# Optimization experiments

Hardware: AMD Instinct MI355X
Metric: run time of the kernel (lower is better)

## Reference

```python
import jax, jax.numpy as jnp
import numpy as np

D = 16          # input_dim
H = 64          # hidden per tiny h-model
HG = 64 * D     # hidden of joint g model = 1024
B = 32768       # batch


def _init_linear(key, out_dim, in_dim):
    # torch nn.Linear default init: U(-1/sqrt(in), 1/sqrt(in)) for W and b
    kw, kb = jax.random.split(key)
    bound = 1.0 / np.sqrt(in_dim)
    W = jax.random.uniform(kw, (out_dim, in_dim), minval=-bound, maxval=bound, dtype=jnp.float32)
    b = jax.random.uniform(kb, (out_dim,), minval=-bound, maxval=bound, dtype=jnp.float32)
    return W, b


def setup_inputs() -> dict:
    key = jax.random.key(0)
    keys = jax.random.split(key, 16)
    x = jax.random.normal(keys[0], (B, 2 * D), dtype=jnp.float32)

    # Stacked weights for the D tiny h-models (1->64->64->64->64->1)
    def stack_h(k, out_dim, in_dim):
        ks = jax.random.split(k, D)
        Ws, bs = [], []
        for kk in ks:
            W, b = _init_linear(kk, out_dim, in_dim)
            Ws.append(W); bs.append(b)
        return jnp.stack(Ws), jnp.stack(bs)

    hW1, hb1 = stack_h(keys[1], H, 1)    # [D,64,1], [D,64]
    hW2, hb2 = stack_h(keys[2], H, H)    # [D,64,64]
    hW3, hb3 = stack_h(keys[3], H, H)
    hW4, hb4 = stack_h(keys[4], H, H)
    hW5, hb5 = stack_h(keys[5], 1, H)    # [D,1,64], [D,1]

    gW1, gb1 = _init_linear(keys[6], HG, D)
    gW2, gb2 = _init_linear(keys[7], HG, HG)
    gW3, gb3 = _init_linear(keys[8], HG, HG)
    gW4, gb4 = _init_linear(keys[9], HG, HG)
    gW5, gb5 = _init_linear(keys[10], 1, HG)

    return {
        "x": x,
        "hW1": hW1, "hb1": hb1, "hW2": hW2, "hb2": hb2,
        "hW3": hW3, "hb3": hb3, "hW4": hW4, "hb4": hb4,
        "hW5": hW5, "hb5": hb5,
        "gW1": gW1, "gb1": gb1, "gW2": gW2, "gb2": gb2,
        "gW3": gW3, "gb3": gb3, "gW4": gW4, "gb4": gb4,
        "gW5": gW5, "gb5": gb5,
    }


def reference(x, hW1, hb1, hW2, hb2, hW3, hb3, hW4, hb4, hW5, hb5,
              gW1, gb1, gW2, gb2, gW3, gb3, gW4, gb4, gW5, gb5):
    first_half = x[:, :D]    # [B, D] -> g branch
    second_half = x[:, D:]   # [B, D] -> D tiny h models, one scalar each

    # --- h branch: D independent 1->64->64->64->64->1 MLPs, batched ---
    # layer 1: scalar input per model; hW1[...,0] has shape [D, H]
    h = jax.nn.relu(second_half[:, :, None] * hW1[:, :, 0][None] + hb1[None])  # [B, D, H]
    h = jax.nn.relu(jnp.einsum('bdh,dgh->bdg', h, hW2) + hb2[None])            # [B, D, H]
    h = jax.nn.relu(jnp.einsum('bdh,dgh->bdg', h, hW3) + hb3[None])
    h = jax.nn.relu(jnp.einsum('bdh,dgh->bdg', h, hW4) + hb4[None])
    outputs_h = jnp.einsum('bdh,doh->bdo', h, hW5)[:, :, 0] + hb5[None, :, 0]  # [B, D]

    # --- g branch: D -> 64D -> ... -> 1 MLP ---
    g = jax.nn.relu(first_half @ gW1.T + gb1)  # [B, HG]
    g = jax.nn.relu(g @ gW2.T + gb2)
    g = jax.nn.relu(g @ gW3.T + gb3)
    g = jax.nn.relu(g @ gW4.T + gb4)
    outputs_g = g @ gW5.T + gb5                # [B, 1]

    return outputs_h, outputs_g
```

## Files before the change

### kernel.cpp

```cpp
#include <hip/hip_runtime.h>

#define B_ROWS 32768
#define D_NETS 16
#define MWH    1048576
#define GW1OFF (3 * MWH)
#define HPOFF  (GW1OFF + 16384)

typedef _Float16 half8 __attribute__((ext_vector_type(8)));
typedef _Float16 half4 __attribute__((ext_vector_type(4)));
typedef __attribute__((ext_vector_type(16))) float f32x16;

#define MFMA16 __builtin_amdgcn_mfma_f32_32x32x16_f16

__global__ void pack_f16(const float* __restrict__ gW1,
                         const float* __restrict__ gW2,
                         const float* __restrict__ gW3,
                         const float* __restrict__ gW4,
                         const float* __restrict__ hW2,
                         const float* __restrict__ hW3,
                         const float* __restrict__ hW4,
                         _Float16* __restrict__ ws) {
    const int p = blockIdx.x * 256 + threadIdx.x;
    const float* src;
    size_t dst;
    if (p < 393216) {
        const int lz = p >> 17;
        const int pl = p & 131071;
        const float* W = (lz == 0) ? gW2 : (lz == 1) ? gW3 : gW4;
        const int l = pl & 63, g = (pl >> 6) & 31, ks = pl >> 11;
        src = &W[(size_t)(g * 32 + (l & 31)) * 1024 + ks * 16 + (l >> 5) * 8];
        dst = (size_t)lz * MWH + (size_t)pl * 8;
    } else if (p < 395264) {
        const int q = p - 393216;
        const int l = q & 63, g = q >> 6;
        src = &gW1[(g * 32 + (l & 31)) * 16 + (l >> 5) * 8];
        dst = GW1OFF + (size_t)q * 8;
    } else {
        const int q = p - 395264;
        const int l = q & 63;
        const int sub = (q >> 6) & 7;
        const int ks = sub >> 1, g = sub & 1;
        const int dL = q >> 9;
        const int d = dL / 3, L = dL - d * 3;
        const float* W = (L == 0) ? hW2 : (L == 1) ? hW3 : hW4;
        src = &W[d * 4096 + (g * 32 + (l & 31)) * 64 + ks * 16 + (l >> 5) * 8];
        dst = HPOFF + (size_t)q * 8;
    }
    half8 v;
    #pragma unroll
    for (int kk = 0; kk < 8; ++kk) v[kk] = (_Float16)src[kk];
    *(half8*)&ws[dst] = v;
}

__global__ __launch_bounds__(256, 4) void h_net_mfma(
    const float* __restrict__ x,
    const float* __restrict__ hW1, const float* __restrict__ hb1,
    const float* __restrict__ hb2, const float* __restrict__ hb3,
    const float* __restrict__ hb4,
    const float* __restrict__ hW5, const float* __restrict__ hb5,
    const _Float16* __restrict__ ws,
    float* __restrict__ out)
{
    __shared__ _Float16 sA[8192];
    __shared__ float s_w1[64], s_b1[64], s_bs[3][64], s_w5[64];

    const int t = threadIdx.x;
    const int d = blockIdx.y;
    const int row0 = blockIdx.x * 128;
    const int l = t & 63, wv = t >> 6;
    const int l31 = l & 31, lk = l >> 5;

    if (t < 64) {
        s_w1[t]    = hW1[d * 64 + t];
        s_b1[t]    = hb1[d * 64 + t];
        s_bs[0][t] = hb2[d * 64 + t];
        s_bs[1][t] = hb3[d * 64 + t];
        s_bs[2][t] = hb4[d * 64 + t];
        s_w5[t]    = hW5[d * 64 + t];
    }
    __syncthreads();

    {
        const int row = t >> 1, jh = t & 1, rg = row >> 5, r31 = row & 31;
        const float sv = x[(size_t)(row0 + row) * 32 + 16 + d];
        #pragma unroll
        for (int jj = 0; jj < 32; ++jj) {
            const int j = jh * 32 + jj;
            const float a = fmaxf(fmaf(sv, s_w1[j], s_b1[j]), 0.f);
            const int ks = j >> 4;
            const int li = ((((j >> 3) & 1) << 5) | r31) ^ (ks << 3);
            sA[((rg * 4 + ks) * 64 + li) * 8 + (j & 7)] = (_Float16)a;
        }
    }
    __syncthreads();

    const _Float16* hp = ws + HPOFF + (size_t)d * 3 * 4096;

    #pragma unroll 1
    for (int L = 0; L < 3; ++L) {
        const _Float16* W = hp + (size_t)L * 4096;
        half8 B[4][2], A[4];
        #pragma unroll
        for (int ks = 0; ks < 4; ++ks) {
            B[ks][0] = *(const half8*)&W[((ks * 2 + 0) * 64 + l) * 8];
            B[ks][1] = *(const half8*)&W[((ks * 2 + 1) * 64 + l) * 8];
            A[ks] = *(const half8*)&sA[((wv * 4 + ks) * 64 + (l ^ (ks << 3))) * 8];
        }
        f32x16 acc[2];
        #pragma unroll
        for (int nt = 0; nt < 2; ++nt) {
            const float bv = s_bs[L][nt * 32 + l31];
            #pragma unroll
            for (int r = 0; r < 16; ++r) acc[nt][r] = bv;
        }
        #pragma unroll
        for (int ks = 0; ks < 4; ++ks) {
            acc[0] = MFMA16(A[ks], B[ks][0], acc[0], 0, 0, 0);
            acc[1] = MFMA16(A[ks], B[ks][1], acc[1], 0, 0, 0);
        }
        __syncthreads();
        #pragma unroll
        for (int nt = 0; nt < 2; ++nt) {
            #pragma unroll
            for (int r = 0; r < 16; ++r) {
                const int r31 = (r & 3) + 8 * (r >> 2) + 4 * lk;
                const int col = nt * 32 + l31;
                const float v = fmaxf(acc[nt][r], 0.f);
                const int ks = col >> 4;
                const int li = ((((col >> 3) & 1) << 5) | r31) ^ (ks << 3);
                sA[((wv * 4 + ks) * 64 + li) * 8 + (col & 7)] = (_Float16)v;
            }
        }
        __syncthreads();
    }

    {
        const int row = t >> 1, jh = t & 1, rg = row >> 5, r31 = row & 31;
        float s = 0.f;
        #pragma unroll
        for (int ks2 = 0; ks2 < 2; ++ks2) {
            const int ks = jh * 2 + ks2;
            #pragma unroll
            for (int h2 = 0; h2 < 2; ++h2) {
                const int li = ((h2 << 5) | r31) ^ (ks << 3);
                half8 v = *(const half8*)&sA[((rg * 4 + ks) * 64 + li) * 8];
                const float* w = &s_w5[ks * 16 + h2 * 8];
                #pragma unroll
                for (int kk = 0; kk < 8; ++kk)
                    s = fmaf((float)v[kk], w[kk], s);
            }
        }
        s += __shfl_xor(s, 1);
        if (jh == 0) out[(size_t)(row0 + row) * 16 + d] = s + hb5[d];
    }
}

__global__ __launch_bounds__(1024, 4) void g_fused_v3(
    const float* __restrict__ x,
    const _Float16* __restrict__ ws,
    const float* __restrict__ gb1, const float* __restrict__ gb2,
    const float* __restrict__ gb3, const float* __restrict__ gb4,
    const float* __restrict__ gW5, const float* __restrict__ gb5,
    float* __restrict__ out)
{
    __shared__ _Float16 sA[65536];
    __shared__ float s_w5f[1024];
    __shared__ float s_red[1024];

    const int t = threadIdx.x;
    const int l = t & 63, wv = t >> 6;
    const int l31 = l & 31, lk = l >> 5;
    const int n0 = wv * 64;
    const int row0 = blockIdx.x * 64;

    s_w5f[t] = gW5[t];

    f32x16 acc[2][2];

#define G_EPI()                                                              \
    {                                                                        \
        _Pragma("unroll")                                                    \
        for (int nt = 0; nt < 2; ++nt) {                                     \
            _Pragma("unroll")                                                \
            for (int rg = 0; rg < 2; ++rg) {                                 \
                _Pragma("unroll")                                            \
                for (int q = 0; q < 4; ++q) {                                \
                    half4 v;                                                 \
                    _Pragma("unroll")                                        \
                    for (int j = 0; j < 4; ++j)                              \
                        v[j] = (_Float16)fmaxf(acc[nt][rg][q * 4 + j], 0.f); \
                    const int ksn = wv * 4 + nt * 2 + (q >> 1);              \
                    const int li  = ((q & 1) << 5) | l31;                    \
                    *(half4*)&sA[((rg * 64 + ksn) * 64 + li) * 8 + lk * 4] = v; \
                }                                                            \
            }                                                                \
        }                                                                    \
    }

    {
        half8 xb[2];
        #pragma unroll
        for (int rg = 0; rg < 2; ++rg) {
            const float* xp = &x[(size_t)(row0 + rg * 32 + l31) * 32 + lk * 8];
            #pragma unroll
            for (int kk = 0; kk < 8; ++kk) xb[rg][kk] = (_Float16)xp[kk];
        }
        #pragma unroll
        for (int nt = 0; nt < 2; ++nt) {
            half8 wb = *(const half8*)&ws[GW1OFF + ((wv * 2 + nt) * 64 + l) * 8];
            #pragma unroll
            for (int rg = 0; rg < 2; ++rg) {
                #pragma unroll
                for (int r = 0; r < 16; ++r)
                    acc[nt][rg][r] =
                        gb1[n0 + nt * 32 + (r & 3) + 8 * (r >> 2) + 4 * lk];
                acc[nt][rg] = MFMA16(wb, xb[rg], acc[nt][rg], 0, 0, 0);
            }
        }
    }
    G_EPI();
    __syncthreads();

#define G_LA(ks, A_)                                                         \
    { A_[0] = *(const half8*)&sA[((ks) * 64 + l) * 8];                       \
      A_[1] = *(const half8*)&sA[((64 + (ks)) * 64 + l) * 8]; }
#define G_LB(ks, B_)                                                         \
    { const int _o = (ks) * 16384 + wv * 1024 + l * 8;                       \
      B_[0] = *(const half8*)&W[_o];                                         \
      B_[1] = *(const half8*)&W[_o + 512]; }
#define G_MM(A_, B_)                                                         \
    { acc[0][0] = MFMA16(B_[0], A_[0], acc[0][0], 0, 0, 0);                  \
      acc[0][1] = MFMA16(B_[0], A_[1], acc[0][1], 0, 0, 0);                  \
      acc[1][0] = MFMA16(B_[1], A_[0], acc[1][0], 0, 0, 0);                  \
      acc[1][1] = MFMA16(B_[1], A_[1], acc[1][1], 0, 0, 0); }

    #pragma unroll 1
    for (int L = 0; L < 3; ++L) {
        const _Float16* W = ws + (size_t)L * MWH;
        const float* gbL = (L == 0) ? gb2 : (L == 1) ? gb3 : gb4;

        half8 A0[2], A1[2], B0[2], B1[2];
        G_LA(0, A0); G_LB(0, B0);
        G_LA(1, A1); G_LB(1, B1);

        #pragma unroll
        for (int nt = 0; nt < 2; ++nt)
            #pragma unroll
            for (int rg = 0; rg < 2; ++rg)
                #pragma unroll
                for (int r = 0; r < 16; ++r)
                    acc[nt][rg][r] =
                        gbL[n0 + nt * 32 + (r & 3) + 8 * (r >> 2) + 4 * lk];

        #pragma unroll 1
        for (int ks = 0; ks < 64; ks += 2) {
            G_MM(A0, B0);
            if (ks + 2 < 64) { G_LA(ks + 2, A0); G_LB(ks + 2, B0); }
            G_MM(A1, B1);
            if (ks + 3 < 64) { G_LA(ks + 3, A1); G_LB(ks + 3, B1); }
        }

        __syncthreads();
        G_EPI();
        __syncthreads();
    }
#undef G_LA
#undef G_LB
#undef G_MM
#undef G_EPI

    {
        const int row = t & 63;
        const int rg5 = row >> 5, r31 = row & 31;
        const int c = t >> 6;
        float s = 0.f;
        #pragma unroll
        for (int q = 0; q < 4; ++q) {
            #pragma unroll
            for (int kh = 0; kh < 2; ++kh) {
                half8 v = *(const half8*)&sA[((rg5 * 64 + c * 4 + q) * 64 +
                                             ((kh << 5) | r31)) * 8];
                const float* w = &s_w5f[(c * 4 + q) * 16 + kh * 8];
                #pragma unroll
                for (int kk = 0; kk < 8; ++kk)
                    s = fmaf((float)v[kk], w[kk], s);
            }
        }
        s_red[t] = s;
    }
    __syncthreads();
    if (t < 64) {
        float s = gb5[0];
        #pragma unroll
        for (int c = 0; c < 16; ++c) s += s_red[c * 64 + t];
        out[(size_t)B_ROWS * D_NETS + row0 + t] = s;
    }
}

extern "C" void kernel_launch(void* const* d_in, const int* in_sizes, int n_in,
                              void* d_out, int out_size, void* d_ws, size_t ws_size,
                              hipStream_t stream) {
    (void)in_sizes; (void)n_in; (void)out_size; (void)ws_size;

    const float* x   = (const float*)d_in[0];
    const float* hW1 = (const float*)d_in[1];
    const float* hb1 = (const float*)d_in[2];
    const float* hW2 = (const float*)d_in[3];
    const float* hb2 = (const float*)d_in[4];
    const float* hW3 = (const float*)d_in[5];
    const float* hb3 = (const float*)d_in[6];
    const float* hW4 = (const float*)d_in[7];
    const float* hb4 = (const float*)d_in[8];
    const float* hW5 = (const float*)d_in[9];
    const float* hb5 = (const float*)d_in[10];
    const float* gW1 = (const float*)d_in[11];
    const float* gb1 = (const float*)d_in[12];
    const float* gW2 = (const float*)d_in[13];
    const float* gb2 = (const float*)d_in[14];
    const float* gW3 = (const float*)d_in[15];
    const float* gb3 = (const float*)d_in[16];
    const float* gW4 = (const float*)d_in[17];
    const float* gb4 = (const float*)d_in[18];
    const float* gW5 = (const float*)d_in[19];
    const float* gb5 = (const float*)d_in[20];
    float* out = (float*)d_out;
    _Float16* wsh = (_Float16*)d_ws;

    pack_f16<<<1640, 256, 0, stream>>>(gW1, gW2, gW3, gW4, hW2, hW3, hW4, wsh);

    dim3 gh(B_ROWS / 128, D_NETS);
    h_net_mfma<<<gh, 256, 0, stream>>>(x, hW1, hb1, hb2, hb3, hb4,
                                       hW5, hb5, wsh, out);

    g_fused_v3<<<B_ROWS / 64, 1024, 0, stream>>>(x, wsh, gb1, gb2, gb3, gb4,
                                                 gW5, gb5, out);
}
```

Measured before the change: 264.0 us.

## Halve g-kernel block to 512 threads with 128-column warp tiles and deeper prefetch

The fused g-MLP kernel now runs 8 waves per block instead of 16. Each wave owns 128 output columns, so it holds 4x2 MFMA accumulators, and each A fragment loaded from LDS feeds twice as many MFMAs. The K-loop becomes a 4-stage rotating register pipeline that prefetches B weights three steps ahead, with clamped indices to avoid branches. This cuts LDS traffic per MFMA and hides global weight-load latency, at the cost of more registers per thread and fewer waves to hide latency.

```diff
diff --git a/kernel.cpp b/kernel.cpp
--- a/kernel.cpp
+++ b/kernel.cpp
@@ -155,7 +155,7 @@
     }
 }
 
-__global__ __launch_bounds__(1024, 4) void g_fused_v3(
+__global__ __launch_bounds__(512, 2) void g_fused_v4(
     const float* __restrict__ x,
     const _Float16* __restrict__ ws,
     const float* __restrict__ gb1, const float* __restrict__ gb2,
@@ -165,22 +165,23 @@
 {
     __shared__ _Float16 sA[65536];
     __shared__ float s_w5f[1024];
-    __shared__ float s_red[1024];
+    __shared__ float s_red[512];
 
     const int t = threadIdx.x;
     const int l = t & 63, wv = t >> 6;
     const int l31 = l & 31, lk = l >> 5;
-    const int n0 = wv * 64;
+    const int n0 = wv * 128;
     const int row0 = blockIdx.x * 64;
 
     s_w5f[t] = gW5[t];
-
-    f32x16 acc[2][2];
+    s_w5f[t + 512] = gW5[t + 512];
+
+    f32x16 acc[4][2];
 
 #define G_EPI()                                                              \
     {                                                                        \
         _Pragma("unroll")                                                    \
-        for (int nt = 0; nt < 2; ++nt) {                                     \
+        for (int nt = 0; nt < 4; ++nt) {                                     \
             _Pragma("unroll")                                                \
             for (int rg = 0; rg < 2; ++rg) {                                 \
                 _Pragma("unroll")                                            \
@@ -189,7 +190,7 @@
                     _Pragma("unroll")                                        \
                     for (int j = 0; j < 4; ++j)                              \
                         v[j] = (_Float16)fmaxf(acc[nt][rg][q * 4 + j], 0.f); \
-                    const int ksn = wv * 4 + nt * 2 + (q >> 1);              \
+                    const int ksn = wv * 8 + nt * 2 + (q >> 1);              \
                     const int li  = ((q & 1) << 5) | l31;                    \
                     *(half4*)&sA[((rg * 64 + ksn) * 64 + li) * 8 + lk * 4] = v; \
                 }                                                            \
@@ -206,8 +207,8 @@
             for (int kk = 0; kk < 8; ++kk) xb[rg][kk] = (_Float16)xp[kk];
         }
         #pragma unroll
-        for (int nt = 0; nt < 2; ++nt) {
-            half8 wb = *(const half8*)&ws[GW1OFF + ((wv * 2 + nt) * 64 + l) * 8];
+        for (int nt = 0; nt < 4; ++nt) {
+            half8 wb = *(const half8*)&ws[GW1OFF + ((wv * 4 + nt) * 64 + l) * 8];
             #pragma unroll
             for (int rg = 0; rg < 2; ++rg) {
                 #pragma unroll
@@ -225,26 +226,31 @@
     { A_[0] = *(const half8*)&sA[((ks) * 64 + l) * 8];                       \
       A_[1] = *(const half8*)&sA[((64 + (ks)) * 64 + l) * 8]; }
 #define G_LB(ks, B_)                                                         \
-    { const int _o = (ks) * 16384 + wv * 1024 + l * 8;                       \
+    { const int _o = (ks) * 16384 + wv * 2048 + l * 8;                       \
       B_[0] = *(const half8*)&W[_o];                                         \
-      B_[1] = *(const half8*)&W[_o + 512]; }
+      B_[1] = *(const half8*)&W[_o + 512];                                   \
+      B_[2] = *(const half8*)&W[_o + 1024];                                  \
+      B_[3] = *(const half8*)&W[_o + 1536]; }
 #define G_MM(A_, B_)                                                         \
-    { acc[0][0] = MFMA16(B_[0], A_[0], acc[0][0], 0, 0, 0);                  \
-      acc[0][1] = MFMA16(B_[0], A_[1], acc[0][1], 0, 0, 0);                  \
-      acc[1][0] = MFMA16(B_[1], A_[0], acc[1][0], 0, 0, 0);                  \
-      acc[1][1] = MFMA16(B_[1], A_[1], acc[1][1], 0, 0, 0); }
+    { _Pragma("unroll")                                                      \
+      for (int nt = 0; nt < 4; ++nt) {                                       \
+          acc[nt][0] = MFMA16(B_[nt], A_[0], acc[nt][0], 0, 0, 0);           \
+          acc[nt][1] = MFMA16(B_[nt], A_[1], acc[nt][1], 0, 0, 0);           \
+      } }
 
     #pragma unroll 1
     for (int L = 0; L < 3; ++L) {
         const _Float16* W = ws + (size_t)L * MWH;
         const float* gbL = (L == 0) ? gb2 : (L == 1) ? gb3 : gb4;
 
-        half8 A0[2], A1[2], B0[2], B1[2];
-        G_LA(0, A0); G_LB(0, B0);
-        G_LA(1, A1); G_LB(1, B1);
-
-        #pragma unroll
-        for (int nt = 0; nt < 2; ++nt)
+        half8 A0[2], A1[2], A2[2], A3[2];
+        half8 B0[4], B1[4], B2[4], B3[4];
+
+        G_LB(0, B0); G_LB(1, B1); G_LB(2, B2);
+        G_LA(0, A0); G_LA(1, A1);
+
+        #pragma unroll
+        for (int nt = 0; nt < 4; ++nt)
             #pragma unroll
             for (int rg = 0; rg < 2; ++rg)
                 #pragma unroll
@@ -253,11 +259,17 @@
                         gbL[n0 + nt * 32 + (r & 3) + 8 * (r >> 2) + 4 * lk];
 
         #pragma unroll 1
-        for (int ks = 0; ks < 64; ks += 2) {
-            G_MM(A0, B0);
-            if (ks + 2 < 64) { G_LA(ks + 2, A0); G_LB(ks + 2, B0); }
-            G_MM(A1, B1);
-            if (ks + 3 < 64) { G_LA(ks + 3, A1); G_LB(ks + 3, B1); }
+        for (int ks = 0; ks < 64; ks += 4) {
+            int s2 = ks + 2; s2 = s2 > 63 ? 63 : s2;
+            int s3 = ks + 3; s3 = s3 > 63 ? 63 : s3;
+            int s4 = ks + 4; s4 = s4 > 63 ? 63 : s4;
+            int s5 = ks + 5; s5 = s5 > 63 ? 63 : s5;
+            int s6 = ks + 6; s6 = s6 > 63 ? 63 : s6;
+
+            G_LB(s3, B3);  G_LA(s2, A2);  G_MM(A0, B0);
+            G_LB(s4, B0);  G_LA(s3, A3);  G_MM(A1, B1);
+            G_LB(s5, B1);  G_LA(s4, A0);  G_MM(A2, B2);
+            G_LB(s6, B2);  G_LA(s5, A1);  G_MM(A3, B3);
         }
 
         __syncthreads();
@@ -270,17 +282,18 @@
 #undef G_EPI
 
     {
-        const int row = t & 63;
+        const int row = l;
         const int rg5 = row >> 5, r31 = row & 31;
-        const int c = t >> 6;
+        const int c = wv;
         float s = 0.f;
         #pragma unroll
-        for (int q = 0; q < 4; ++q) {
+        for (int q = 0; q < 8; ++q) {
+            const int ksn = c * 8 + q;
             #pragma unroll
             for (int kh = 0; kh < 2; ++kh) {
-                half8 v = *(const half8*)&sA[((rg5 * 64 + c * 4 + q) * 64 +
+                half8 v = *(const half8*)&sA[((rg5 * 64 + ksn) * 64 +
                                              ((kh << 5) | r31)) * 8];
-                const float* w = &s_w5f[(c * 4 + q) * 16 + kh * 8];
+                const float* w = &s_w5f[ksn * 16 + kh * 8];
                 #pragma unroll
                 for (int kk = 0; kk < 8; ++kk)
                     s = fmaf((float)v[kk], w[kk], s);
@@ -292,7 +305,7 @@
     if (t < 64) {
         float s = gb5[0];
         #pragma unroll
-        for (int c = 0; c < 16; ++c) s += s_red[c * 64 + t];
+        for (int c = 0; c < 8; ++c) s += s_red[c * 64 + t];
         out[(size_t)B_ROWS * D_NETS + row0 + t] = s;
     }
 }
@@ -332,6 +345,6 @@
     h_net_mfma<<<gh, 256, 0, stream>>>(x, hW1, hb1, hb2, hb3, hb4,
                                        hW5, hb5, wsh, out);
 
-    g_fused_v3<<<B_ROWS / 64, 1024, 0, stream>>>(x, wsh, gb1, gb2, gb3, gb4,
-                                                 gW5, gb5, out);
+    g_fused_v4<<<B_ROWS / 64, 512, 0, stream>>>(x, wsh, gb1, gb2, gb3, gb4,
+                                                gW5, gb5, out);
 }
```

Result: slower. 390.7 us (+48.0%).

## Deepen weight prefetch pipeline across layers and raise MFMA issue priority

Applied to the files above, without the earlier changes.

Rewrites the g-branch hidden-layer inner loop to keep three global weight fragments in flight instead of one. The k-loop is fully unrolled in steps of four, and the prefetch crosses layer boundaries, fetching the next layer's first weight tiles while the current layer finishes. MFMA groups are wrapped in s_setprio to favour matrix issue over memory ops. The extra live half8 registers raise register pressure at 1024 threads per block, and the full unroll grows code size.

```diff
diff --git a/kernel.cpp b/kernel.cpp
--- a/kernel.cpp
+++ b/kernel.cpp
@@ -155,7 +155,7 @@
     }
 }
 
-__global__ __launch_bounds__(1024, 4) void g_fused_v3(
+__global__ __launch_bounds__(1024, 4) void g_fused_v5(
     const float* __restrict__ x,
     const _Float16* __restrict__ ws,
     const float* __restrict__ gb1, const float* __restrict__ gb2,
@@ -176,6 +176,17 @@
     s_w5f[t] = gW5[t];
 
     f32x16 acc[2][2];
+    half8 A0[2], A1[2], A2[2], A3[2];
+    half8 B0[2], B1[2], B2[2], B3[2];
+
+#define G_LBP(W_, ks, B_)                                                    \
+    { const int _o = (ks) * 16384 + wv * 1024 + l * 8;                       \
+      B_[0] = *(const half8*)&W_[_o];                                        \
+      B_[1] = *(const half8*)&W_[_o + 512]; }
+
+    G_LBP(ws, 0, B0);
+    G_LBP(ws, 1, B1);
+    G_LBP(ws, 2, B2);
 
 #define G_EPI()                                                              \
     {                                                                        \
@@ -224,24 +235,25 @@
 #define G_LA(ks, A_)                                                         \
     { A_[0] = *(const half8*)&sA[((ks) * 64 + l) * 8];                       \
       A_[1] = *(const half8*)&sA[((64 + (ks)) * 64 + l) * 8]; }
-#define G_LB(ks, B_)                                                         \
-    { const int _o = (ks) * 16384 + wv * 1024 + l * 8;                       \
-      B_[0] = *(const half8*)&W[_o];                                         \
-      B_[1] = *(const half8*)&W[_o + 512]; }
+#define G_LAC(ks, A_)  { if ((ks) <= 63) G_LA(ks, A_) }
+#define G_LBX(s, B_)                                                         \
+    { if ((s) > 63) { G_LBP(Wn, (s) & 63, B_) } else { G_LBP(W, s, B_) } }
 #define G_MM(A_, B_)                                                         \
-    { acc[0][0] = MFMA16(B_[0], A_[0], acc[0][0], 0, 0, 0);                  \
+    { __builtin_amdgcn_s_setprio(1);                                         \
+      acc[0][0] = MFMA16(B_[0], A_[0], acc[0][0], 0, 0, 0);                  \
       acc[0][1] = MFMA16(B_[0], A_[1], acc[0][1], 0, 0, 0);                  \
       acc[1][0] = MFMA16(B_[1], A_[0], acc[1][0], 0, 0, 0);                  \
-      acc[1][1] = MFMA16(B_[1], A_[1], acc[1][1], 0, 0, 0); }
+      acc[1][1] = MFMA16(B_[1], A_[1], acc[1][1], 0, 0, 0);                  \
+      __builtin_amdgcn_s_setprio(0); }
 
     #pragma unroll 1
     for (int L = 0; L < 3; ++L) {
-        const _Float16* W = ws + (size_t)L * MWH;
+        const _Float16* W  = ws + (size_t)L * MWH;
+        const _Float16* Wn = ws + (size_t)(L < 2 ? L + 1 : L) * MWH;
         const float* gbL = (L == 0) ? gb2 : (L == 1) ? gb3 : gb4;
 
-        half8 A0[2], A1[2], B0[2], B1[2];
-        G_LA(0, A0); G_LB(0, B0);
-        G_LA(1, A1); G_LB(1, B1);
+        G_LA(0, A0);
+        G_LA(1, A1);
 
         #pragma unroll
         for (int nt = 0; nt < 2; ++nt)
@@ -252,12 +264,12 @@
                     acc[nt][rg][r] =
                         gbL[n0 + nt * 32 + (r & 3) + 8 * (r >> 2) + 4 * lk];
 
-        #pragma unroll 1
-        for (int ks = 0; ks < 64; ks += 2) {
-            G_MM(A0, B0);
-            if (ks + 2 < 64) { G_LA(ks + 2, A0); G_LB(ks + 2, B0); }
-            G_MM(A1, B1);
-            if (ks + 3 < 64) { G_LA(ks + 3, A1); G_LB(ks + 3, B1); }
+        #pragma unroll
+        for (int ks = 0; ks < 64; ks += 4) {
+            G_LBX(ks + 3, B3);  G_LAC(ks + 2, A2);  G_MM(A0, B0);
+            G_LBX(ks + 4, B0);  G_LAC(ks + 3, A3);  G_MM(A1, B1);
+            G_LBX(ks + 5, B1);  G_LAC(ks + 4, A0);  G_MM(A2, B2);
+            G_LBX(ks + 6, B2);  G_LAC(ks + 5, A1);  G_MM(A3, B3);
         }
 
         __syncthreads();
@@ -265,7 +277,9 @@
         __syncthreads();
     }
 #undef G_LA
-#undef G_LB
+#undef G_LAC
+#undef G_LBX
+#undef G_LBP
 #undef G_MM
 #undef G_EPI
 
@@ -332,6 +346,6 @@
     h_net_mfma<<<gh, 256, 0, stream>>>(x, hW1, hb1, hb2, hb3, hb4,
                                        hW5, hb5, wsh, out);
 
-    g_fused_v3<<<B_ROWS / 64, 1024, 0, stream>>>(x, wsh, gb1, gb2, gb3, gb4,
+    g_fused_v5<<<B_ROWS / 64, 1024, 0, stream>>>(x, wsh, gb1, gb2, gb3, gb4,
                                                  gW5, gb5, out);
 }
```

After: 342.5 us. 29.7% more time.
